# Kernel tuning notes

Hardware: AMD Instinct MI355X
Metric: run time of the kernel (lower is better)

The kernel has to match this reference:

```python
import jax, jax.numpy as jnp
import numpy as np

B, N, IN_DIM = 16, 2048, 64
DIM, HEADS, DEPTH, K, NCLS = 512, 8, 4, 256, 2
DH = DIM // HEADS
EPS = 1e-5


def layernorm(h, s, b):
    mu = jnp.mean(h, axis=-1, keepdims=True)
    var = jnp.mean(jnp.square(h - mu), axis=-1, keepdims=True)
    return (h - mu) * jax.lax.rsqrt(var + EPS) * s + b


def setup_inputs() -> dict:
    key = jax.random.key(0)
    ks = jax.random.split(key, 20)
    w = 0.02
    L = DEPTH
    return {
        "x": jax.random.normal(ks[0], (B, N, IN_DIM), jnp.float32),
        "emb_w": jax.random.normal(ks[1], (IN_DIM, DIM), jnp.float32) * w,
        "emb_b": jnp.zeros((DIM,), jnp.float32),
        "pos": jax.random.normal(ks[2], (1, N, DIM), jnp.float32) * w,
        "ln1_s": jnp.ones((L, DIM), jnp.float32),
        "ln1_b": jnp.zeros((L, DIM), jnp.float32),
        "wq": jax.random.normal(ks[3], (L, DIM, DIM), jnp.float32) * w,
        "wk": jax.random.normal(ks[4], (L, DIM, DIM), jnp.float32) * w,
        "wv": jax.random.normal(ks[5], (L, DIM, DIM), jnp.float32) * w,
        "pk": jax.random.normal(ks[6], (L, N, K), jnp.float32) * (1.0 / np.sqrt(N)),
        "pv": jax.random.normal(ks[7], (L, N, K), jnp.float32) * (1.0 / np.sqrt(N)),
        "wo": jax.random.normal(ks[8], (L, DIM, DIM), jnp.float32) * w,
        "wo_b": jnp.zeros((L, DIM), jnp.float32),
        "ln2_s": jnp.ones((L, DIM), jnp.float32),
        "ln2_b": jnp.zeros((L, DIM), jnp.float32),
        "w1": jax.random.normal(ks[9], (L, DIM, 4 * DIM), jnp.float32) * w,
        "b1": jnp.zeros((L, 4 * DIM), jnp.float32),
        "w2": jax.random.normal(ks[10], (L, 4 * DIM, DIM), jnp.float32) * w,
        "b2": jnp.zeros((L, DIM), jnp.float32),
        "fc_w": jax.random.normal(ks[11], (DIM, NCLS), jnp.float32) * w,
        "fc_b": jnp.zeros((NCLS,), jnp.float32),
    }


def reference(x, emb_w, emb_b, pos, ln1_s, ln1_b, wq, wk, wv, pk, pv, wo, wo_b,
              ln2_s, ln2_b, w1, b1, w2, b2, fc_w, fc_b):
    scale = DH ** -0.5
    h = x @ emb_w + emb_b + pos  # [B,N,DIM]
    for i in range(DEPTH):
        # Linformer self-attention (PreNorm + residual)
        z = layernorm(h, ln1_s[i], ln1_b[i])
        q = (z @ wq[i]).reshape(B, N, HEADS, DH)
        k = z @ wk[i]  # [B,N,DIM]
        v = z @ wv[i]
        # low-rank projection along sequence: [B,N,DIM] x [N,K] -> [B,K,DIM]
        kp = jnp.einsum('bnd,nk->bkd', k, pk[i]).reshape(B, K, HEADS, DH)
        vp = jnp.einsum('bnd,nk->bkd', v, pv[i]).reshape(B, K, HEADS, DH)
        dots = jnp.einsum('bnhd,bkhd->bhnk', q, kp) * scale
        attn = jax.nn.softmax(dots, axis=-1)
        out = jnp.einsum('bhnk,bkhd->bnhd', attn, vp).reshape(B, N, DIM)
        h = h + out @ wo[i] + wo_b[i]
        # FeedForward (PreNorm + residual)
        z = layernorm(h, ln2_s[i], ln2_b[i])
        h = h + jax.nn.gelu(z @ w1[i] + b1[i]) @ w2[i] + b2[i]
    pooled = jnp.mean(h, axis=1)  # [B,DIM]
    return pooled @ fc_w + fc_b  # [B,NCLS]
```

## Files before the change

kernel.cpp:

```cpp
#include <hip/hip_runtime.h>
#include <math.h>

#define B_    16
#define N_    2048
#define INDIM 64
#define DIM_  512
#define HEADS 8
#define DEPTH 4
#define KLIN  256
#define NCLS  2
#define DH    64
#define EPSF  1e-5f

typedef __attribute__((ext_vector_type(8))) short short8v;
typedef __attribute__((ext_vector_type(4))) short short4v;
typedef __attribute__((ext_vector_type(4))) float f32x4;

__device__ __forceinline__ short f2bf(float f) {
  unsigned u = __float_as_uint(f);
  u += 0x7FFFu + ((u >> 16) & 1u);
  return (short)(u >> 16);
}

__device__ __forceinline__ float wave_sum(float v) {
  #pragma unroll
  for (int o = 32; o > 0; o >>= 1) v += __shfl_xor(v, o);
  return v;
}

__device__ __forceinline__ float gelu_tanh(float x) {
  float u = x * (1.5957691216057308f + 0.07135481627f * x * x);
  return x / (1.f + __expf(-u));
}

__device__ __forceinline__ void gl_lds16(const short* g, short* l) {
  __builtin_amdgcn_global_load_lds(
      (const __attribute__((address_space(1))) unsigned int*)g,
      (__attribute__((address_space(3))) unsigned int*)l, 16, 0, 0);
}

__global__ __launch_bounds__(256) void tconv_k(const float* __restrict__ src,
                                               short* __restrict__ dst, int R,
                                               int C, long long sSrc,
                                               long long sDst) {
  __shared__ float tile[32][33];
  int c0 = blockIdx.x * 32, r0 = blockIdx.y * 32;
  src += (long long)blockIdx.z * sSrc;
  dst += (long long)blockIdx.z * sDst;
  int tx = threadIdx.x & 31, ty = threadIdx.x >> 5;
  #pragma unroll
  for (int rr = 0; rr < 4; ++rr)
    tile[ty + rr * 8][tx] = src[(long long)(r0 + ty + rr * 8) * C + c0 + tx];
  __syncthreads();
  #pragma unroll
  for (int rr = 0; rr < 4; ++rr) {
    int c = ty + rr * 8;
    dst[(long long)(c0 + c) * R + r0 + tx] = f2bf(tile[tx][c]);
  }
}

__global__ __launch_bounds__(256) void cconv_k(const float* __restrict__ src,
                                               short* __restrict__ dst,
                                               int n8) {
  int i = blockIdx.x * 256 + threadIdx.x;
  if (i < n8) {
    const float* s = src + (long long)i * 8;
    float4 a = *(const float4*)s, c = *(const float4*)(s + 4);
    short8v o = {f2bf(a.x), f2bf(a.y), f2bf(a.z), f2bf(a.w),
                 f2bf(c.x), f2bf(c.y), f2bf(c.z), f2bf(c.w)};
    *(short8v*)(dst + (long long)i * 8) = o;
  }
}

__global__ __launch_bounds__(256) void tpose_k(const short* __restrict__ src,
                                               short* __restrict__ dst, int R,
                                               int C, long long sSrc,
                                               long long sDst) {
  __shared__ __align__(16) short tile[64][72];
  int c0 = blockIdx.x * 64, r0 = blockIdx.y * 64;
  src += (long long)blockIdx.z * sSrc;
  dst += (long long)blockIdx.z * sDst;
  int t = threadIdx.x;
  #pragma unroll
  for (int rep = 0; rep < 2; ++rep) {
    int row = rep * 32 + (t >> 3), c8 = (t & 7) * 8;
    *(short8v*)&tile[row][c8] =
        *(const short8v*)(src + (long long)(r0 + row) * C + c0 + c8);
  }
  __syncthreads();
  #pragma unroll
  for (int rep = 0; rep < 2; ++rep) {
    int c = rep * 32 + (t >> 3), r8 = (t & 7) * 8;
    short8v o;
    #pragma unroll
    for (int j = 0; j < 8; ++j) o[j] = tile[r8 + j][c];
    *(short8v*)(dst + (long long)(c0 + c) * R + r0 + r8) = o;
  }
}

__global__ __launch_bounds__(256) void ln_k(const float* __restrict__ h,
                                            const float* __restrict__ s,
                                            const float* __restrict__ b,
                                            short* __restrict__ z) {
  int lane = threadIdx.x & 63;
  long long row = ((long long)blockIdx.x << 2) + (threadIdx.x >> 6);
  const float* hr = h + row * DIM_ + lane * 8;
  float4 a = *(const float4*)hr;
  float4 c = *(const float4*)(hr + 4);
  float sum = a.x + a.y + a.z + a.w + c.x + c.y + c.z + c.w;
  sum = wave_sum(sum);
  float mu = sum * (1.f / DIM_);
  float d[8] = {a.x - mu, a.y - mu, a.z - mu, a.w - mu,
                c.x - mu, c.y - mu, c.z - mu, c.w - mu};
  float vs = 0.f;
  #pragma unroll
  for (int i = 0; i < 8; ++i) vs += d[i] * d[i];
  vs = wave_sum(vs);
  float rstd = rsqrtf(vs * (1.f / DIM_) + EPSF);
  const float* sp = s + lane * 8;
  const float* bp = b + lane * 8;
  float4 s0 = *(const float4*)sp, s1 = *(const float4*)(sp + 4);
  float4 b0 = *(const float4*)bp, b1 = *(const float4*)(bp + 4);
  float o[8];
  o[0] = d[0] * rstd * s0.x + b0.x; o[1] = d[1] * rstd * s0.y + b0.y;
  o[2] = d[2] * rstd * s0.z + b0.z; o[3] = d[3] * rstd * s0.w + b0.w;
  o[4] = d[4] * rstd * s1.x + b1.x; o[5] = d[5] * rstd * s1.y + b1.y;
  o[6] = d[6] * rstd * s1.z + b1.z; o[7] = d[7] * rstd * s1.w + b1.w;
  short8v ov = {f2bf(o[0]), f2bf(o[1]), f2bf(o[2]), f2bf(o[3]),
                f2bf(o[4]), f2bf(o[5]), f2bf(o[6]), f2bf(o[7])};
  *(short8v*)(z + row * DIM_ + lane * 8) = ov;
}

template <int OUTBF, int BM, int BN>
__global__ __launch_bounds__(256) void gemm_bf(
    const short* __restrict__ A, const short* __restrict__ Bsrc,
    const float* __restrict__ bias, const float* __restrict__ resid,
    void* __restrict__ Cv, int M, int N, int K, int lda, int ldb, int ldc,
    long long sAb, long long sBb, long long sCb, int dualThresh,
    long long dualOff, int epi, int resMod) {
  constexpr int MT = BM / 32;
  constexpr int NT = BN / 32;
  constexpr int NLD = BM / 32 + BN / 32;
  int zz = blockIdx.z;
  A += (long long)zz * sAb;
  Bsrc += (long long)zz * sBb;
  int bm = blockIdx.y * BM, bn = blockIdx.x * BN;
  if (dualThresh && bm >= dualThresh) Bsrc += dualOff;
  int t = threadIdx.x;
  __shared__ __align__(16) short Alds[2][BM * 64];
  __shared__ __align__(16) short Blds[2][BN * 64];
  int lane = t & 63, wid = t >> 6;
  int lr = lane & 15, q = lane >> 4;
  int wm = (wid >> 1) * (BM / 2), wn = (wid & 1) * (BN / 2);
  int rl = lane >> 3;
  int cs = (lane & 7) ^ rl;
  f32x4 acc[MT][NT] = {};

  auto stage = [&](int buf, int k0) {
    #pragma unroll
    for (int i = 0; i < BM / 32; ++i) {
      int rb = i * 32 + wid * 8;
      gl_lds16(A + (long long)(bm + rb + rl) * lda + k0 + cs * 8,
               &Alds[buf][rb * 64]);
    }
    #pragma unroll
    for (int i = 0; i < BN / 32; ++i) {
      int rb = i * 32 + wid * 8;
      gl_lds16(Bsrc + (long long)(bn + rb + rl) * ldb + k0 + cs * 8,
               &Blds[buf][rb * 64]);
    }
  };

  stage(0, 0);
  int cur = 0;
  for (int k0 = 0; k0 < K; k0 += 64, cur ^= 1) {
    if (k0 + 64 < K) {
      stage(cur ^ 1, k0 + 64);
      __builtin_amdgcn_sched_barrier(0);
      asm volatile("s_waitcnt vmcnt(%0)" ::"n"(NLD) : "memory");
    } else {
      __builtin_amdgcn_sched_barrier(0);
      asm volatile("s_waitcnt vmcnt(0)" ::: "memory");
    }
    __builtin_amdgcn_s_barrier();
    __builtin_amdgcn_sched_barrier(0);
    #pragma unroll
    for (int kk2 = 0; kk2 < 2; ++kk2) {
      short8v af[MT], bfr[NT];
      #pragma unroll
      for (int mi = 0; mi < MT; ++mi)
        af[mi] = *(const short8v*)&Alds[cur][(wm + mi * 16 + lr) * 64 +
                                             (((kk2 << 2) | q) ^ (lr & 7)) * 8];
      #pragma unroll
      for (int ni = 0; ni < NT; ++ni)
        bfr[ni] = *(const short8v*)&Blds[cur][(wn + ni * 16 + lr) * 64 +
                                              (((kk2 << 2) | q) ^ (lr & 7)) * 8];
      #pragma unroll
      for (int mi = 0; mi < MT; ++mi)
        #pragma unroll
        for (int ni = 0; ni < NT; ++ni)
          acc[mi][ni] = __builtin_amdgcn_mfma_f32_16x16x32_bf16(
              bfr[ni], af[mi], acc[mi][ni], 0, 0, 0);
    }
    __builtin_amdgcn_sched_barrier(0);
    __builtin_amdgcn_s_barrier();
  }

  #pragma unroll
  for (int mi = 0; mi < MT; ++mi) {
    int m = bm + wm + mi * 16 + lr;
    int rm = (epi == 2 && resMod) ? (m % resMod) : m;
    #pragma unroll
    for (int ni = 0; ni < NT; ++ni) {
      int nb = bn + wn + ni * 16 + q * 4;
      f32x4 v = acc[mi][ni];
      if (epi >= 1) {
        float4 bb = *(const float4*)(bias + nb);
        v[0] += bb.x; v[1] += bb.y; v[2] += bb.z; v[3] += bb.w;
      }
      if (epi == 2) {
        float4 rr = *(const float4*)(resid + (long long)rm * ldc + nb);
        v[0] += rr.x; v[1] += rr.y; v[2] += rr.z; v[3] += rr.w;
      } else if (epi == 3) {
        v[0] = gelu_tanh(v[0]); v[1] = gelu_tanh(v[1]);
        v[2] = gelu_tanh(v[2]); v[3] = gelu_tanh(v[3]);
      }
      long long base = (long long)zz * sCb + (long long)m * ldc + nb;
      if (OUTBF) {
        short4v o = {f2bf(v[0]), f2bf(v[1]), f2bf(v[2]), f2bf(v[3])};
        *(short4v*)((short*)Cv + base) = o;
      } else {
        *(float4*)((float*)Cv + base) = make_float4(v[0], v[1], v[2], v[3]);
      }
    }
  }
}

__global__ __launch_bounds__(256) void attn_k(short* __restrict__ qc,
                                              const short* __restrict__ kvp,
                                              float scale) {
  int n0 = blockIdx.x * 64, hh = blockIdx.y, b = blockIdx.z;
  int t = threadIdx.x;
  int lane = t & 63, w = t >> 6;
  int lr = lane & 15, qd = lane >> 4;

  __shared__ __align__(16) short Qlds[64][72];
  __shared__ __align__(16) short Kbuf[256 * 72];
  __shared__ __align__(16) short Vt[64][264];
  auto Klds = (short(*)[72])Kbuf;
  auto Plds = (short(*)[264])Kbuf;

  short* qptr = qc + (long long)b * N_ * DIM_ + hh * DH;
  const short* kptr = kvp + (long long)b * 2 * KLIN * DIM_ + hh * DH;
  const short* vptr = kptr + (long long)KLIN * DIM_;

  #pragma unroll
  for (int rep = 0; rep < 2; ++rep) {
    int L = rep * 256 + t, row = L >> 3, c8 = (L & 7) << 3;
    *(short8v*)&Qlds[row][c8] =
        *(const short8v*)(qptr + (long long)(n0 + row) * DIM_ + c8);
  }
  #pragma unroll
  for (int rep = 0; rep < 8; ++rep) {
    int L = rep * 256 + t, row = L >> 3, c8 = (L & 7) << 3;
    *(short8v*)&Klds[row][c8] =
        *(const short8v*)(kptr + (long long)row * DIM_ + c8);
  }
  #pragma unroll
  for (int rep = 0; rep < 4; ++rep) {
    int key0 = rep * 64 + (t >> 4) * 4, dh0 = (t & 15) * 4;
    short4v a0 = *(const short4v*)(vptr + (long long)(key0 + 0) * DIM_ + dh0);
    short4v a1 = *(const short4v*)(vptr + (long long)(key0 + 1) * DIM_ + dh0);
    short4v a2 = *(const short4v*)(vptr + (long long)(key0 + 2) * DIM_ + dh0);
    short4v a3 = *(const short4v*)(vptr + (long long)(key0 + 3) * DIM_ + dh0);
    short4v w0 = {a0[0], a1[0], a2[0], a3[0]};
    short4v w1 = {a0[1], a1[1], a2[1], a3[1]};
    short4v w2 = {a0[2], a1[2], a2[2], a3[2]};
    short4v w3 = {a0[3], a1[3], a2[3], a3[3]};
    *(short4v*)&Vt[dh0 + 0][key0] = w0;
    *(short4v*)&Vt[dh0 + 1][key0] = w1;
    *(short4v*)&Vt[dh0 + 2][key0] = w2;
    *(short4v*)&Vt[dh0 + 3][key0] = w3;
  }
  __syncthreads();

  short8v qa0 = *(const short8v*)&Qlds[16 * w + lr][qd * 8];
  short8v qa1 = *(const short8v*)&Qlds[16 * w + lr][32 + qd * 8];
  f32x4 sacc[16];
  #pragma unroll
  for (int nt = 0; nt < 16; ++nt) {
    short8v b0 = *(const short8v*)&Klds[nt * 16 + lr][qd * 8];
    short8v b1 = *(const short8v*)&Klds[nt * 16 + lr][32 + qd * 8];
    f32x4 acc = {};
    acc = __builtin_amdgcn_mfma_f32_16x16x32_bf16(qa0, b0, acc, 0, 0, 0);
    acc = __builtin_amdgcn_mfma_f32_16x16x32_bf16(qa1, b1, acc, 0, 0, 0);
    sacc[nt] = acc;
  }

  #pragma unroll
  for (int r = 0; r < 4; ++r) {
    float m = -1e30f;
    #pragma unroll
    for (int nt = 0; nt < 16; ++nt) {
      sacc[nt][r] *= scale;
      m = fmaxf(m, sacc[nt][r]);
    }
    #pragma unroll
    for (int o = 1; o < 16; o <<= 1) m = fmaxf(m, __shfl_xor(m, o));
    float rs = 0.f;
    #pragma unroll
    for (int nt = 0; nt < 16; ++nt) {
      float e = __expf(sacc[nt][r] - m);
      sacc[nt][r] = e;
      rs += e;
    }
    #pragma unroll
    for (int o = 1; o < 16; o <<= 1) rs += __shfl_xor(rs, o);
    float inv = 1.f / rs;
    #pragma unroll
    for (int nt = 0; nt < 16; ++nt) sacc[nt][r] *= inv;
  }

  __syncthreads();
  #pragma unroll
  for (int nt = 0; nt < 16; ++nt)
    #pragma unroll
    for (int r = 0; r < 4; ++r)
      Plds[16 * w + qd * 4 + r][nt * 16 + lr] = f2bf(sacc[nt][r]);
  __syncthreads();

  f32x4 out[4] = {};
  #pragma unroll
  for (int k0 = 0; k0 < 8; ++k0) {
    short8v ap = *(const short8v*)&Plds[16 * w + lr][k0 * 32 + qd * 8];
    #pragma unroll
    for (int n2 = 0; n2 < 4; ++n2) {
      short8v bv = *(const short8v*)&Vt[n2 * 16 + lr][k0 * 32 + qd * 8];
      out[n2] =
          __builtin_amdgcn_mfma_f32_16x16x32_bf16(bv, ap, out[n2], 0, 0, 0);
    }
  }

  long long rowoff = (long long)(n0 + 16 * w + lr) * DIM_;
  #pragma unroll
  for (int n2 = 0; n2 < 4; ++n2) {
    short4v o = {f2bf(out[n2][0]), f2bf(out[n2][1]), f2bf(out[n2][2]),
                 f2bf(out[n2][3])};
    *(short4v*)(qptr + rowoff + n2 * 16 + qd * 4) = o;
  }
}

__global__ __launch_bounds__(256) void pool1_k(const float* __restrict__ h,
                                               float* __restrict__ partial) {
  int stripe = blockIdx.x, b = blockIdx.y;
  int c4 = (threadIdx.x & 127) * 4, half = threadIdx.x >> 7;
  const float* base =
      h + ((long long)b * N_ + stripe * 128 + half * 64) * DIM_ + c4;
  float4 acc = {0.f, 0.f, 0.f, 0.f};
  for (int r = 0; r < 64; ++r) {
    float4 v = *(const float4*)(base + (long long)r * DIM_);
    acc.x += v.x; acc.y += v.y; acc.z += v.z; acc.w += v.w;
  }
  __shared__ float red[512];
  if (half == 1) *(float4*)&red[c4] = acc;
  __syncthreads();
  if (half == 0) {
    float4 o = *(const float4*)&red[c4];
    o.x += acc.x; o.y += acc.y; o.z += acc.z; o.w += acc.w;
    *(float4*)&partial[((long long)b * 16 + stripe) * DIM_ + c4] = o;
  }
}
__global__ __launch_bounds__(256) void pool2_k(const float* __restrict__ partial,
                                               float* __restrict__ pooled) {
  int b = blockIdx.x;
  for (int c = threadIdx.x; c < DIM_; c += 256) {
    float s = 0.f;
    for (int k = 0; k < 16; ++k) s += partial[((long long)b * 16 + k) * DIM_ + c];
    pooled[b * DIM_ + c] = s * (1.f / N_);
  }
}

__global__ __launch_bounds__(64) void fc_k(const float* __restrict__ pooled,
                                           const float* __restrict__ fc_w,
                                           const float* __restrict__ fc_b,
                                           float* __restrict__ out) {
  int t = threadIdx.x;
  if (t < B_ * NCLS) {
    int b = t >> 1, c = t & 1;
    float s = fc_b[c];
    for (int d = 0; d < DIM_; ++d)
      s += pooled[b * DIM_ + d] * fc_w[d * NCLS + c];
    out[t] = s;
  }
}

extern "C" void kernel_launch(void* const* d_in, const int* in_sizes, int n_in,
                              void* d_out, int out_size, void* d_ws,
                              size_t ws_size, hipStream_t stream) {
  const float* x     = (const float*)d_in[0];
  const float* emb_w = (const float*)d_in[1];
  const float* emb_b = (const float*)d_in[2];
  const float* pos   = (const float*)d_in[3];
  const float* ln1_s = (const float*)d_in[4];
  const float* ln1_b = (const float*)d_in[5];
  const float* wq    = (const float*)d_in[6];
  const float* wk    = (const float*)d_in[7];
  const float* wv    = (const float*)d_in[8];
  const float* pk    = (const float*)d_in[9];
  const float* pv    = (const float*)d_in[10];
  const float* wo    = (const float*)d_in[11];
  const float* wo_b  = (const float*)d_in[12];
  const float* ln2_s = (const float*)d_in[13];
  const float* ln2_b = (const float*)d_in[14];
  const float* w1    = (const float*)d_in[15];
  const float* b1    = (const float*)d_in[16];
  const float* w2    = (const float*)d_in[17];
  const float* b2    = (const float*)d_in[18];
  const float* fc_w  = (const float*)d_in[19];
  const float* fc_b  = (const float*)d_in[20];
  float* out = (float*)d_out;

  const bool big = ws_size >= (size_t)230 * 1024 * 1024;
  const int acb = big ? 16 : 8;
  const long long acrows = (long long)acb * N_;
  const int frows = big ? 16384 : 8192;

  char* P = (char*)d_ws;
  float* h = (float*)P;            P += (long long)B_ * N_ * DIM_ * 4;
  short* zc = (short*)P;           P += acrows * DIM_ * 2;
  short* qc = (short*)P;           P += acrows * DIM_ * 2;
  short* ffnmid = zc;
  short* zcT = (short*)P;          P += acrows * DIM_ * 2;
  short* zln = zcT;
  short* zp = (short*)P;           P += (long long)acb * 2 * KLIN * DIM_ * 2;
  short* kvp = (short*)P;          P += (long long)acb * 2 * KLIN * DIM_ * 2;
  short* wq_t  = (short*)P;  P += (long long)DEPTH * DIM_ * DIM_ * 2;
  short* wkv_t = (short*)P;  P += (long long)DEPTH * 2 * DIM_ * DIM_ * 2;
  short* wo_t  = (short*)P;  P += (long long)DEPTH * DIM_ * DIM_ * 2;
  short* w1_t  = (short*)P;  P += (long long)DEPTH * 4 * DIM_ * DIM_ * 2;
  short* w2_t  = (short*)P;  P += (long long)DEPTH * 4 * DIM_ * DIM_ * 2;
  short* pkv_t = (short*)P;  P += (long long)DEPTH * 2 * KLIN * N_ * 2;
  short* emb_wt = (short*)P; P += (long long)DIM_ * INDIM * 2;
  short* x_bf  = (short*)P;  P += (long long)B_ * N_ * INDIM * 2;
  float* partial = (float*)P; P += (long long)B_ * 16 * DIM_ * 4;
  float* pooled  = (float*)P;

  const float scale = 0.125f;
  const long long WQS = (long long)DIM_ * DIM_;
  const long long KVS = (long long)2 * KLIN * DIM_;

  auto tconv = [&](const float* s, short* d, int R, int C, long long ss,
                   long long sd, int b) {
    hipLaunchKernelGGL(tconv_k, dim3(C / 32, R / 32, b), dim3(256), 0, stream,
                       s, d, R, C, ss, sd);
  };
  tconv(wq, wq_t, DIM_, DIM_, WQS, WQS, DEPTH);
  tconv(wk, wkv_t, DIM_, DIM_, WQS, 2 * WQS, DEPTH);
  tconv(wv, wkv_t + WQS, DIM_, DIM_, WQS, 2 * WQS, DEPTH);
  tconv(wo, wo_t, DIM_, DIM_, WQS, WQS, DEPTH);
  tconv(w1, w1_t, DIM_, 4 * DIM_, 4 * WQS, 4 * WQS, DEPTH);
  tconv(w2, w2_t, 4 * DIM_, DIM_, 4 * WQS, 4 * WQS, DEPTH);
  tconv(pk, pkv_t, N_, KLIN, (long long)N_ * KLIN, (long long)2 * KLIN * N_, DEPTH);
  tconv(pv, pkv_t + (long long)KLIN * N_, N_, KLIN, (long long)N_ * KLIN,
        (long long)2 * KLIN * N_, DEPTH);
  tconv(emb_w, emb_wt, INDIM, DIM_, 0, 0, 1);
  hipLaunchKernelGGL(cconv_k, dim3((B_ * N_ * INDIM / 8 + 255) / 256),
                     dim3(256), 0, stream, x, x_bf, B_ * N_ * INDIM / 8);

  hipLaunchKernelGGL((gemm_bf<0, 128, 128>), dim3(DIM_ / 128, B_ * N_ / 128, 1),
                     dim3(256), 0, stream, x_bf, emb_wt, emb_b, pos, (void*)h,
                     B_ * N_, DIM_, INDIM, INDIM, INDIM, DIM_, 0LL, 0LL, 0LL,
                     0, 0LL, 2, N_);

  for (int i = 0; i < DEPTH; ++i) {
    const short* wq_i  = wq_t + i * WQS;
    const short* wkv_i = wkv_t + i * 2 * WQS;
    const short* wo_i  = wo_t + i * WQS;
    const short* w1_i  = w1_t + (long long)i * 4 * WQS;
    const short* w2_i  = w2_t + (long long)i * 4 * WQS;
    const short* pkv_i = pkv_t + (long long)i * 2 * KLIN * N_;

    for (int c = 0; c < B_ / acb; ++c) {
      float* hc = h + (long long)c * acrows * DIM_;
      hipLaunchKernelGGL(ln_k, dim3(acrows / 4), dim3(256), 0, stream, hc,
                         ln1_s + i * DIM_, ln1_b + i * DIM_, zc);
      hipLaunchKernelGGL(tpose_k, dim3(DIM_ / 64, N_ / 64, acb), dim3(256), 0,
                         stream, zc, zcT, N_, DIM_, (long long)N_ * DIM_,
                         (long long)DIM_ * N_);
      hipLaunchKernelGGL((gemm_bf<1, 64, 256>), dim3(DIM_ / 256, acrows / 64, 1),
                         dim3(256), 0, stream, zc, wq_i, nullptr, nullptr,
                         (void*)qc, (int)acrows, DIM_, DIM_, DIM_, DIM_, DIM_,
                         0LL, 0LL, 0LL, 0, 0LL, 0, 0);
      hipLaunchKernelGGL((gemm_bf<1, 64, 128>), dim3(DIM_ / 128, 512 / 64, acb),
                         dim3(256), 0, stream, pkv_i, zcT, nullptr, nullptr,
                         (void*)zp, 512, DIM_, N_, N_, N_, DIM_, 0LL,
                         (long long)DIM_ * N_, KVS, 0, 0LL, 0, 0);
      hipLaunchKernelGGL((gemm_bf<1, 64, 128>), dim3(DIM_ / 128, 512 / 64, acb),
                         dim3(256), 0, stream, zp, wkv_i, nullptr, nullptr,
                         (void*)kvp, 512, DIM_, DIM_, DIM_, DIM_, DIM_, KVS,
                         0LL, KVS, KLIN, (long long)WQS, 0, 0);
      hipLaunchKernelGGL(attn_k, dim3(N_ / 64, HEADS, acb), dim3(256), 0,
                         stream, qc, kvp, scale);
      hipLaunchKernelGGL((gemm_bf<0, 64, 256>), dim3(DIM_ / 256, acrows / 64, 1),
                         dim3(256), 0, stream, qc, wo_i, wo_b + i * DIM_,
                         hc, (void*)hc, (int)acrows, DIM_, DIM_, DIM_, DIM_,
                         DIM_, 0LL, 0LL, 0LL, 0, 0LL, 2, 0);
    }

    for (int r0 = 0; r0 < B_ * N_; r0 += frows) {
      float* hr = h + (long long)r0 * DIM_;
      hipLaunchKernelGGL(ln_k, dim3(frows / 4), dim3(256), 0, stream, hr,
                         ln2_s + i * DIM_, ln2_b + i * DIM_, zln);
      hipLaunchKernelGGL((gemm_bf<1, 128, 128>),
                         dim3(4 * DIM_ / 128, frows / 128, 1), dim3(256), 0,
                         stream, zln, w1_i, b1 + (long long)i * 4 * DIM_,
                         nullptr, (void*)ffnmid, frows, 4 * DIM_, DIM_, DIM_,
                         DIM_, 4 * DIM_, 0LL, 0LL, 0LL, 0, 0LL, 3, 0);
      hipLaunchKernelGGL((gemm_bf<0, 64, 256>), dim3(DIM_ / 256, frows / 64, 1),
                         dim3(256), 0, stream, ffnmid, w2_i,
                         b2 + (long long)i * DIM_, hr, (void*)hr, frows, DIM_,
                         4 * DIM_, 4 * DIM_, 4 * DIM_, DIM_, 0LL, 0LL, 0LL, 0,
                         0LL, 2, 0);
    }
  }

  hipLaunchKernelGGL(pool1_k, dim3(16, B_), dim3(256), 0, stream, h, partial);
  hipLaunchKernelGGL(pool2_k, dim3(B_), dim3(256), 0, stream, partial, pooled);
  hipLaunchKernelGGL(fc_k, dim3(1), dim3(64), 0, stream, pooled, fc_w, fc_b,
                     out);
}
```

Baseline: 2.142 ms.

## Add 8-wave 256-row GEMM with interleaved LDS staging for projection and FFN GEMMs

Adds a new GEMM kernel using 512 threads (8 waves) and 256-row tiles. Each K-step is split into four MFMA quarter-phases, with global-to-LDS prefetches of the next tiles interleaved between them, plus barriers and s_setprio to favour the MFMA waves. The Q, output-projection and both FFN GEMMs switch to this kernel to get more reuse per loaded tile and better overlap of loads with matrix math. The larger tiles mean fewer blocks per launch, which may lower occupancy or leave parts of the device idle on the smaller GEMMs, and it raises register and LDS pressure.

```diff
diff --git a/kernel.cpp b/kernel.cpp
--- a/kernel.cpp
+++ b/kernel.cpp
@@ -15,6 +15,8 @@
 typedef __attribute__((ext_vector_type(8))) short short8v;
 typedef __attribute__((ext_vector_type(4))) short short4v;
 typedef __attribute__((ext_vector_type(4))) float f32x4;
+
+#define SBAR() __builtin_amdgcn_sched_barrier(0)
 
 __device__ __forceinline__ short f2bf(float f) {
   unsigned u = __float_as_uint(f);
@@ -176,14 +178,14 @@
   for (int k0 = 0; k0 < K; k0 += 64, cur ^= 1) {
     if (k0 + 64 < K) {
       stage(cur ^ 1, k0 + 64);
-      __builtin_amdgcn_sched_barrier(0);
+      SBAR();
       asm volatile("s_waitcnt vmcnt(%0)" ::"n"(NLD) : "memory");
     } else {
-      __builtin_amdgcn_sched_barrier(0);
+      SBAR();
       asm volatile("s_waitcnt vmcnt(0)" ::: "memory");
     }
     __builtin_amdgcn_s_barrier();
-    __builtin_amdgcn_sched_barrier(0);
+    SBAR();
     #pragma unroll
     for (int kk2 = 0; kk2 < 2; ++kk2) {
       short8v af[MT], bfr[NT];
@@ -202,7 +204,7 @@
           acc[mi][ni] = __builtin_amdgcn_mfma_f32_16x16x32_bf16(
               bfr[ni], af[mi], acc[mi][ni], 0, 0, 0);
     }
-    __builtin_amdgcn_sched_barrier(0);
+    SBAR();
     __builtin_amdgcn_s_barrier();
   }
 
@@ -226,6 +228,175 @@
         v[2] = gelu_tanh(v[2]); v[3] = gelu_tanh(v[3]);
       }
       long long base = (long long)zz * sCb + (long long)m * ldc + nb;
+      if (OUTBF) {
+        short4v o = {f2bf(v[0]), f2bf(v[1]), f2bf(v[2]), f2bf(v[3])};
+        *(short4v*)((short*)Cv + base) = o;
+      } else {
+        *(float4*)((float*)Cv + base) = make_float4(v[0], v[1], v[2], v[3]);
+      }
+    }
+  }
+}
+
+template <int OUTBF, int BN, int EPI>
+__global__ __launch_bounds__(512, 2) void gemm8(
+    const short* __restrict__ A, const short* __restrict__ Bt,
+    const float* __restrict__ bias, const float* __restrict__ resid,
+    void* __restrict__ Cv, int M, int N, int K) {
+  constexpr int BM = 256;
+  constexpr int WCOL = BN / 4;
+  constexpr int NT = WCOL / 16;
+  constexpr int NTH = NT / 2;
+  constexpr int LB = BN / 128;
+  __shared__ __align__(16) short Alds[2][BM * 64];
+  __shared__ __align__(16) short Blds[2][BN * 64];
+  const int tid = threadIdx.x;
+  const int lane = tid & 63, wid = tid >> 6;
+  const int lr = lane & 15, q = lane >> 4;
+  const int wm = (wid >> 2) * 128, wn = (wid & 3) * WCOL;
+  const int rl = lane >> 3, cs = (lane & 7) ^ rl;
+  const int bm = blockIdx.y * BM, bn = blockIdx.x * BN;
+  const short* Ag = A + (long long)bm * K + cs * 8;
+  const short* Bg = Bt + (long long)bn * K + cs * 8;
+  f32x4 acc[8][NT] = {};
+
+  auto stageA = [&](int slot, int h, int k0) {
+    #pragma unroll
+    for (int j = 0; j < 2; ++j) {
+      int rb = h * 128 + j * 64 + wid * 8;
+      gl_lds16(Ag + (long long)(rb + rl) * K + k0, &Alds[slot][rb * 64]);
+    }
+  };
+  auto stageB = [&](int slot, int h, int k0) {
+    #pragma unroll
+    for (int j = 0; j < LB; ++j) {
+      int rb = h * (BN / 2) + j * 64 + wid * 8;
+      gl_lds16(Bg + (long long)(rb + rl) * K + k0, &Blds[slot][rb * 64]);
+    }
+  };
+  auto rd = [&](const short* Ls, int row, int kk) -> short8v {
+    return *(const short8v*)&Ls[row * 64 + ((((kk << 2) | q) ^ (lr & 7)) << 3)];
+  };
+  auto mfma4 = [&](short8v (&af)[4][2], short8v (&bf)[NTH][2], int mo, int no) {
+    #pragma unroll
+    for (int mi = 0; mi < 4; ++mi)
+      #pragma unroll
+      for (int ni = 0; ni < NTH; ++ni)
+        #pragma unroll
+        for (int kk = 0; kk < 2; ++kk)
+          acc[mo + mi][no + ni] = __builtin_amdgcn_mfma_f32_16x16x32_bf16(
+              bf[ni][kk], af[mi][kk], acc[mo + mi][no + ni], 0, 0, 0);
+  };
+
+  const int T = K >> 6;
+  stageA(0, 0, 0); stageA(0, 1, 0); stageB(0, 0, 0); stageB(0, 1, 0);
+  if (T > 1) {
+    stageA(1, 0, 64);
+    SBAR();
+    asm volatile("s_waitcnt vmcnt(2)" ::: "memory");
+  } else {
+    SBAR();
+    asm volatile("s_waitcnt vmcnt(0)" ::: "memory");
+  }
+  __builtin_amdgcn_s_barrier();
+
+  for (int tt = 0; tt < T; ++tt) {
+    const int s = tt & 1, ns = s ^ 1;
+    const int kn = (tt + 1) << 6, kn2 = (tt + 2) << 6;
+    const short* Als = Alds[s];
+    const short* Bls = Blds[s];
+    short8v af0[4][2], af1[4][2], bf0[NTH][2], bf1[NTH][2];
+    SBAR();
+    #pragma unroll
+    for (int mi = 0; mi < 4; ++mi)
+      #pragma unroll
+      for (int kk = 0; kk < 2; ++kk)
+        af0[mi][kk] = rd(Als, wm + mi * 16 + lr, kk);
+    #pragma unroll
+    for (int ni = 0; ni < NTH; ++ni)
+      #pragma unroll
+      for (int kk = 0; kk < 2; ++kk)
+        bf0[ni][kk] = rd(Bls, wn + ni * 16 + lr, kk);
+    if (tt + 1 < T) stageA(ns, 1, kn);
+    if (BN == 256) asm volatile("s_waitcnt lgkmcnt(8)" ::: "memory");
+    SBAR();
+    __builtin_amdgcn_s_barrier();
+    asm volatile("s_waitcnt lgkmcnt(0)" ::: "memory");
+    SBAR();
+    __builtin_amdgcn_s_setprio(1);
+    mfma4(af0, bf0, 0, 0);
+    __builtin_amdgcn_s_setprio(0);
+    SBAR();
+    __builtin_amdgcn_s_barrier();
+    SBAR();
+    #pragma unroll
+    for (int ni = 0; ni < NTH; ++ni)
+      #pragma unroll
+      for (int kk = 0; kk < 2; ++kk)
+        bf1[ni][kk] = rd(Bls, wn + (NTH + ni) * 16 + lr, kk);
+    SBAR();
+    __builtin_amdgcn_s_barrier();
+    asm volatile("s_waitcnt lgkmcnt(0)" ::: "memory");
+    SBAR();
+    __builtin_amdgcn_s_setprio(1);
+    mfma4(af0, bf1, 0, NTH);
+    __builtin_amdgcn_s_setprio(0);
+    SBAR();
+    __builtin_amdgcn_s_barrier();
+    SBAR();
+    #pragma unroll
+    for (int mi = 0; mi < 4; ++mi)
+      #pragma unroll
+      for (int kk = 0; kk < 2; ++kk)
+        af1[mi][kk] = rd(Als, wm + 64 + mi * 16 + lr, kk);
+    if (tt + 1 < T) stageB(ns, 0, kn);
+    SBAR();
+    __builtin_amdgcn_s_barrier();
+    asm volatile("s_waitcnt lgkmcnt(0)" ::: "memory");
+    SBAR();
+    __builtin_amdgcn_s_setprio(1);
+    mfma4(af1, bf0, 4, 0);
+    __builtin_amdgcn_s_setprio(0);
+    SBAR();
+    __builtin_amdgcn_s_barrier();
+    SBAR();
+    if (tt + 1 < T) stageB(ns, 1, kn);
+    if (tt + 2 < T) stageA(s, 0, kn2);
+    SBAR();
+    __builtin_amdgcn_s_barrier();
+    __builtin_amdgcn_s_setprio(1);
+    mfma4(af1, bf1, 4, NTH);
+    __builtin_amdgcn_s_setprio(0);
+    if (tt + 2 < T) {
+      SBAR();
+      asm volatile("s_waitcnt vmcnt(2)" ::: "memory");
+    } else if (tt + 1 < T) {
+      SBAR();
+      asm volatile("s_waitcnt vmcnt(0)" ::: "memory");
+    }
+    SBAR();
+    __builtin_amdgcn_s_barrier();
+  }
+
+  #pragma unroll
+  for (int mi = 0; mi < 8; ++mi) {
+    int m = bm + wm + mi * 16 + lr;
+    #pragma unroll
+    for (int nj = 0; nj < NT; ++nj) {
+      int nb = bn + wn + nj * 16 + q * 4;
+      f32x4 v = acc[mi][nj];
+      if (EPI >= 1) {
+        float4 bb = *(const float4*)(bias + nb);
+        v[0] += bb.x; v[1] += bb.y; v[2] += bb.z; v[3] += bb.w;
+      }
+      if (EPI == 2) {
+        float4 rr = *(const float4*)(resid + (long long)m * N + nb);
+        v[0] += rr.x; v[1] += rr.y; v[2] += rr.z; v[3] += rr.w;
+      } else if (EPI == 3) {
+        v[0] = gelu_tanh(v[0]); v[1] = gelu_tanh(v[1]);
+        v[2] = gelu_tanh(v[2]); v[3] = gelu_tanh(v[3]);
+      }
+      long long base = (long long)m * N + nb;
       if (OUTBF) {
         short4v o = {f2bf(v[0]), f2bf(v[1]), f2bf(v[2]), f2bf(v[3])};
         *(short4v*)((short*)Cv + base) = o;
@@ -487,10 +658,10 @@
       hipLaunchKernelGGL(tpose_k, dim3(DIM_ / 64, N_ / 64, acb), dim3(256), 0,
                          stream, zc, zcT, N_, DIM_, (long long)N_ * DIM_,
                          (long long)DIM_ * N_);
-      hipLaunchKernelGGL((gemm_bf<1, 64, 256>), dim3(DIM_ / 256, acrows / 64, 1),
-                         dim3(256), 0, stream, zc, wq_i, nullptr, nullptr,
-                         (void*)qc, (int)acrows, DIM_, DIM_, DIM_, DIM_, DIM_,
-                         0LL, 0LL, 0LL, 0, 0LL, 0, 0);
+      hipLaunchKernelGGL((gemm8<1, 256, 0>),
+                         dim3(DIM_ / 256, (int)(acrows / 256), 1), dim3(512), 0,
+                         stream, zc, wq_i, nullptr, nullptr, (void*)qc,
+                         (int)acrows, DIM_, DIM_);
       hipLaunchKernelGGL((gemm_bf<1, 64, 128>), dim3(DIM_ / 128, 512 / 64, acb),
                          dim3(256), 0, stream, pkv_i, zcT, nullptr, nullptr,
                          (void*)zp, 512, DIM_, N_, N_, N_, DIM_, 0LL,
@@ -501,26 +672,24 @@
                          0LL, KVS, KLIN, (long long)WQS, 0, 0);
       hipLaunchKernelGGL(attn_k, dim3(N_ / 64, HEADS, acb), dim3(256), 0,
                          stream, qc, kvp, scale);
-      hipLaunchKernelGGL((gemm_bf<0, 64, 256>), dim3(DIM_ / 256, acrows / 64, 1),
-                         dim3(256), 0, stream, qc, wo_i, wo_b + i * DIM_,
-                         hc, (void*)hc, (int)acrows, DIM_, DIM_, DIM_, DIM_,
-                         DIM_, 0LL, 0LL, 0LL, 0, 0LL, 2, 0);
+      hipLaunchKernelGGL((gemm8<0, 256, 2>),
+                         dim3(DIM_ / 256, (int)(acrows / 256), 1), dim3(512), 0,
+                         stream, qc, wo_i, wo_b + i * DIM_, hc, (void*)hc,
+                         (int)acrows, DIM_, DIM_);
     }
 
     for (int r0 = 0; r0 < B_ * N_; r0 += frows) {
       float* hr = h + (long long)r0 * DIM_;
       hipLaunchKernelGGL(ln_k, dim3(frows / 4), dim3(256), 0, stream, hr,
                          ln2_s + i * DIM_, ln2_b + i * DIM_, zln);
-      hipLaunchKernelGGL((gemm_bf<1, 128, 128>),
-                         dim3(4 * DIM_ / 128, frows / 128, 1), dim3(256), 0,
+      hipLaunchKernelGGL((gemm8<1, 256, 3>),
+                         dim3(4 * DIM_ / 256, frows / 256, 1), dim3(512), 0,
                          stream, zln, w1_i, b1 + (long long)i * 4 * DIM_,
-                         nullptr, (void*)ffnmid, frows, 4 * DIM_, DIM_, DIM_,
-                         DIM_, 4 * DIM_, 0LL, 0LL, 0LL, 0, 0LL, 3, 0);
-      hipLaunchKernelGGL((gemm_bf<0, 64, 256>), dim3(DIM_ / 256, frows / 64, 1),
-                         dim3(256), 0, stream, ffnmid, w2_i,
-                         b2 + (long long)i * DIM_, hr, (void*)hr, frows, DIM_,
-                         4 * DIM_, 4 * DIM_, 4 * DIM_, DIM_, 0LL, 0LL, 0LL, 0,
-                         0LL, 2, 0);
+                         nullptr, (void*)ffnmid, frows, 4 * DIM_, DIM_);
+      hipLaunchKernelGGL((gemm8<0, 128, 2>),
+                         dim3(DIM_ / 128, frows / 256, 1), dim3(512), 0,
+                         stream, ffnmid, w2_i, b2 + (long long)i * DIM_, hr,
+                         (void*)hr, frows, DIM_, 4 * DIM_);
     }
   }
 
```

New measurement: 1.988 ms. 1.08x faster.
